# Performance work log

Measured on AMD Instinct MI355X. Metric: run time of the kernel, lower is better.

## Reference

```python
import jax, jax.numpy as jnp
import numpy as np

DIM = 384
HEADS = 8


def setup_inputs() -> dict:
    key = jax.random.key(0)
    k_x, k_qkv, k_pw, k_pb = jax.random.split(key, 4)
    x = jax.random.normal(k_x, (8, DIM, 32, 32), dtype=jnp.float32)
    # Conv2d 1x1 weights stored as [out, in]
    w_qkv = jax.random.normal(k_qkv, (3 * DIM, DIM), dtype=jnp.float32) * (DIM ** -0.5)
    w_proj = jax.random.normal(k_pw, (DIM, DIM), dtype=jnp.float32) * (DIM ** -0.5)
    b_proj = jax.random.normal(k_pb, (DIM,), dtype=jnp.float32) * 0.02
    return {"x": x, "w_qkv": w_qkv, "w_proj": w_proj, "b_proj": b_proj}


def reference(x, w_qkv, w_proj, b_proj):
    B, C, H, W = x.shape
    h = HEADS
    d = C // h
    scale = d ** -0.5
    # 1x1 conv == channel-wise linear: [B,3C,H,W]
    qkv = jnp.einsum('oc,bchw->bohw', w_qkv, x)
    q, k, v = jnp.split(qkv, 3, axis=1)
    # B (h d) H W -> B h (H W) d
    def to_heads(y):
        return y.reshape(B, h, d, H * W).transpose(0, 1, 3, 2)
    q, k, v = to_heads(q), to_heads(k), to_heads(v)
    att = jnp.einsum('bhxd,bhyd->bhxy', q * scale, k)
    att = jax.nn.softmax(att, axis=-1)
    out = jnp.einsum('bhxy,bhyd->bhxd', att, v)
    # B h (H W) d -> B (h d) H W
    out = out.transpose(0, 1, 3, 2).reshape(B, C, H, W)
    out = jnp.einsum('oc,bchw->bohw', w_proj, out) + b_proj[None, :, None, None]
    return out
```

## Files before the change

kernel.cpp:

```cpp
#include <hip/hip_runtime.h>
#include <math.h>

typedef unsigned short u16;
typedef __attribute__((ext_vector_type(8))) short short8;
typedef __attribute__((ext_vector_type(8))) unsigned short ushort8;
typedef __attribute__((ext_vector_type(4))) float floatx4;
typedef __attribute__((ext_vector_type(2))) unsigned int uint2v;
typedef __attribute__((ext_vector_type(4))) unsigned int uint4v;

#define SEQ 1024
#define CDIM 384
#define NH 8
#define DH 48
#define DP 64
#define NB 8

__device__ __forceinline__ u16 f2bf(float f){
  unsigned int u; __builtin_memcpy(&u, &f, 4);
  u = (u + 0x7fffu + ((u >> 16) & 1u)) >> 16;
  return (u16)u;
}
__device__ __forceinline__ unsigned cvtpk(float a, float b){
  unsigned r;
  asm("v_cvt_pk_bf16_f32 %0, %1, %2" : "=v"(r) : "v"(a), "v"(b));
  return r;
}
__device__ __forceinline__ void plswap32(unsigned &a, unsigned &b){
  asm("v_permlane32_swap_b32 %0, %1" : "+v"(a), "+v"(b));
}
__device__ __forceinline__ void plswap16(unsigned &a, unsigned &b){
  asm("v_permlane16_swap_b32 %0, %1" : "+v"(a), "+v"(b));
}
__device__ __forceinline__ void async16(const u16* g, u16* l){
  __builtin_amdgcn_global_load_lds((const __attribute__((address_space(1))) void*)g,
                                   (__attribute__((address_space(3))) void*)l, 16, 0, 0);
}

__global__ __launch_bounds__(256) void prep_kernel(const float* __restrict__ x,
                                                   const float* __restrict__ wq,
                                                   const float* __restrict__ wp,
                                                   u16* __restrict__ xT,
                                                   u16* __restrict__ wdst){
  __shared__ u16 ldsT[64 * 72];
  const int id = blockIdx.x;
  const int t = threadIdx.x;
  if (id < 768){
    const int bx = id & 15, by = (id >> 4) % 6, bz = id / 96;
    const int c0 = by * 64;
    const int s0 = bx * 64;
    const int rr = t >> 2, q4 = t & 3;

    const float* src = x + ((size_t)(bz * CDIM + c0 + rr)) * SEQ + s0;
#pragma unroll
    for (int i = 0; i < 4; i++){
      const int cc = q4 + i * 4;
      float4 f = *(const float4*)(src + cc * 4);
      ldsT[(cc * 4 + 0) * 72 + rr] = f2bf(f.x);
      ldsT[(cc * 4 + 1) * 72 + rr] = f2bf(f.y);
      ldsT[(cc * 4 + 2) * 72 + rr] = f2bf(f.z);
      ldsT[(cc * 4 + 3) * 72 + rr] = f2bf(f.w);
    }
    __syncthreads();
    u16* dst = xT + ((size_t)(bz * SEQ + s0 + rr)) * CDIM + c0 + q4 * 16;
    *(ushort8*)(dst)     = *(const ushort8*)&ldsT[rr * 72 + q4 * 16];
    *(ushort8*)(dst + 8) = *(const ushort8*)&ldsT[rr * 72 + q4 * 16 + 8];
  } else {
    const int NWQ = 3 * CDIM * CDIM;
    const int i = ((id - 768) * 256 + t) * 4;
    const float* src = (i < NWQ) ? (wq + i) : (wp + (i - NWQ));
    float4 f = *(const float4*)src;
    uint2v v; v[0] = cvtpk(f.x, f.y); v[1] = cvtpk(f.z, f.w);
    *(uint2v*)(wdst + i) = v;
  }
}

__global__ __launch_bounds__(256) void qkv_kernel(const u16* __restrict__ W,
                                                  const u16* __restrict__ xT,
                                                  u16* __restrict__ qws,
                                                  u16* __restrict__ kws,
                                                  u16* __restrict__ vws){
  __shared__ u16 ldsA[128 * 64];
  __shared__ u16 ldsB[64 * 64];
  const int t = threadIdx.x;
  const int w = t >> 6, l = t & 63;
  const int quad = l >> 4, li = l & 15;
  const int n0 = blockIdx.x * 64;
  const int m0 = blockIdx.y * 128;
  const int b  = blockIdx.z;

  floatx4 acc[2][4];
#pragma unroll
  for (int i = 0; i < 2; i++)
#pragma unroll
    for (int j = 0; j < 4; j++) acc[i][j] = (floatx4)0.0f;

  const u16* xb = xT + (size_t)b * SEQ * CDIM;
  const int swz = li & 7;

  for (int kk = 0; kk < CDIM; kk += 64){
    __syncthreads();
#pragma unroll
    for (int rep = 0; rep < 4; rep++){
      const int cs = rep * 256 + t;
      const int row = cs >> 3, c4 = cs & 7;
      async16(&W[(size_t)(m0 + row) * CDIM + kk + ((c4 ^ (row & 7)) << 3)], &ldsA[cs * 8]);
    }
#pragma unroll
    for (int rep = 0; rep < 2; rep++){
      const int cs = rep * 256 + t;
      const int row = cs >> 3, c4 = cs & 7;
      async16(&xb[(size_t)(n0 + row) * CDIM + kk + ((c4 ^ (row & 7)) << 3)], &ldsB[cs * 8]);
    }
    __syncthreads();
#pragma unroll
    for (int kc = 0; kc < 2; kc++){
      const int rc = ((kc * 4 + quad) ^ swz) << 3;
      short8 af[2], bf[4];
#pragma unroll
      for (int i = 0; i < 2; i++)
        af[i] = *(const short8*)&ldsA[(w * 32 + i * 16 + li) * 64 + rc];
#pragma unroll
      for (int j = 0; j < 4; j++)
        bf[j] = *(const short8*)&ldsB[(j * 16 + li) * 64 + rc];
#pragma unroll
      for (int i = 0; i < 2; i++)
#pragma unroll
        for (int j = 0; j < 4; j++)
          acc[i][j] = __builtin_amdgcn_mfma_f32_16x16x32_bf16(af[i], bf[j], acc[i][j], 0, 0, 0);
    }
  }

  const float qs = 0.14433756729740643f * 1.4426950408889634f;
  const uint2v z2 = (uint2v)0u;
#pragma unroll
  for (int i = 0; i < 2; i++){
    const int obase = m0 + w * 32 + i * 16 + quad * 4;
    const int which = obase / CDIM;
    const int rem = obase - which * CDIM;
    const int h = rem / DH;
    const int dd = rem - h * DH;
    const int pair = b * NH + h;
#pragma unroll
    for (int j = 0; j < 4; j++){
      const int s = n0 + j * 16 + li;
      floatx4 v = acc[i][j];
      if (which == 0){
        uint2v pk; pk[0] = cvtpk(v[0] * qs, v[1] * qs); pk[1] = cvtpk(v[2] * qs, v[3] * qs);
        *(uint2v*)&qws[((size_t)pair * SEQ + s) * DP + dd] = pk;
        if ((dd & 48) == 32)
          *(uint2v*)&qws[((size_t)pair * SEQ + s) * DP + dd + 16] = z2;
      } else if (which == 1){
        uint2v pk; pk[0] = cvtpk(v[0], v[1]); pk[1] = cvtpk(v[2], v[3]);
        *(uint2v*)&kws[((size_t)pair * SEQ + s) * DP + dd] = pk;
        if ((dd & 48) == 32)
          *(uint2v*)&kws[((size_t)pair * SEQ + s) * DP + dd + 16] = z2;
      } else {
#pragma unroll
        for (int r = 0; r < 4; r++)
          vws[((size_t)pair * DH + dd + r) * SEQ + s] = f2bf(v[r]);
      }
    }
  }
}

__global__ __launch_bounds__(256, 4) void attn_kernel(const u16* __restrict__ qws,
                                                      const u16* __restrict__ kws,
                                                      const u16* __restrict__ vws,
                                                      u16* __restrict__ aT){
  __shared__ u16 ldsK[2][64 * 64];
  __shared__ u16 ldsV[2][48 * 64];

  const int t = threadIdx.x;
  const int w = t >> 6, l = t & 63;
  const int quad = l >> 4, li = l & 15;
  const int id = blockIdx.x;
  const int pair = id & 63;
  const int qb = id >> 6;
  const int b = pair >> 3, h = pair & 7;
  const int qbase = qb * 64 + w * 16;
  const int swz = li & 7;

  const u16* qrow = qws + ((size_t)pair * SEQ + qbase + li) * DP;
  const short8 qf0 = *(const short8*)(qrow + quad * 8);
  const short8 qf1 = *(const short8*)(qrow + 32 + quad * 8);

  floatx4 ot[3];
#pragma unroll
  for (int dt = 0; dt < 3; dt++) ot[dt] = (floatx4)0.0f;
  float m_run = -3.0e38f, l_run = 0.0f;

  const u16* kbase = kws + (size_t)pair * SEQ * DP;
  const u16* vbase = vws + (size_t)pair * DH * SEQ;

  auto stage = [&](int kv, int pp){
#pragma unroll
    for (int rep = 0; rep < 4; rep++){
      const int cs = rep * 256 + t;
      if (cs < 512){
        const int row = cs >> 3, c4 = cs & 7;
        async16(&kbase[(size_t)(kv + row) * DP + ((c4 ^ (row & 7)) << 3)],
                &ldsK[pp][cs * 8]);
      } else if (cs < 896){
        const int cs2 = cs - 512;
        const int row = cs2 >> 3, c4 = cs2 & 7;
        async16(&vbase[(size_t)row * SEQ + kv + ((c4 ^ (row & 7)) << 3)],
                &ldsV[pp][cs2 * 8]);
      }
    }
  };

  stage(0, 0);
  for (int i = 0; i < 16; i++){
    const int p = i & 1;
    __syncthreads();
    if (i < 15) stage((i + 1) * 64, p ^ 1);

    floatx4 st[4];
#pragma unroll
    for (int yt = 0; yt < 4; yt++){
      const u16* krow = ldsK[p] + (yt * 16 + li) * 64;
      const short8 kf0 = *(const short8*)(krow + (((0 + quad) ^ swz) << 3));
      const short8 kf1 = *(const short8*)(krow + (((4 + quad) ^ swz) << 3));
      floatx4 z = (floatx4)0.0f;
      z = __builtin_amdgcn_mfma_f32_16x16x32_bf16(kf0, qf0, z, 0, 0, 0);
      z = __builtin_amdgcn_mfma_f32_16x16x32_bf16(kf1, qf1, z, 0, 0, 0);
      st[yt] = z;
    }

    float mx = -3.0e38f;
#pragma unroll
    for (int yt = 0; yt < 4; yt++)
      mx = fmaxf(mx, fmaxf(fmaxf(st[yt][0], st[yt][1]), fmaxf(st[yt][2], st[yt][3])));
    mx = fmaxf(mx, __shfl_xor(mx, 16, 64));
    mx = fmaxf(mx, __shfl_xor(mx, 32, 64));

    if (!__all(mx - m_run <= 11.0f)){
      const float mnew = fmaxf(m_run, mx);
      const float alpha = __builtin_amdgcn_exp2f(m_run - mnew);
      m_run = mnew;
      l_run *= alpha;
#pragma unroll
      for (int dt = 0; dt < 3; dt++) ot[dt] *= alpha;
    }

    unsigned wv[4][2];
    float ls = 0.0f;
#pragma unroll
    for (int yt = 0; yt < 4; yt++){
      float p0 = __builtin_amdgcn_exp2f(st[yt][0] - m_run);
      float p1 = __builtin_amdgcn_exp2f(st[yt][1] - m_run);
      float p2 = __builtin_amdgcn_exp2f(st[yt][2] - m_run);
      float p3 = __builtin_amdgcn_exp2f(st[yt][3] - m_run);
      ls += (p0 + p1) + (p2 + p3);
      wv[yt][0] = cvtpk(p0, p1);
      wv[yt][1] = cvtpk(p2, p3);
    }
    l_run += ls;

#pragma unroll
    for (int kh = 0; kh < 2; kh++){
      unsigned d0 = wv[2 * kh][0],     d1 = wv[2 * kh][1];
      unsigned e0 = wv[2 * kh + 1][0], e1 = wv[2 * kh + 1][1];
      plswap32(d0, e0); plswap16(d0, e0);
      plswap32(d1, e1); plswap16(d1, e1);
      uint4v u; u[0] = d0; u[1] = d1; u[2] = e0; u[3] = e1;
      const short8 pb = __builtin_bit_cast(short8, u);
#pragma unroll
      for (int dt = 0; dt < 3; dt++){
        const short8 vf = *(const short8*)&ldsV[p][(dt * 16 + li) * 64 +
                                                  (((kh * 4 + quad) ^ swz) << 3)];
        ot[dt] = __builtin_amdgcn_mfma_f32_16x16x32_bf16(vf, pb, ot[dt], 0, 0, 0);
      }
    }
  }

  float ls = l_run;
  ls += __shfl_xor(ls, 16, 64);
  ls += __shfl_xor(ls, 32, 64);
  const float rl = __builtin_amdgcn_rcpf(ls);
  const int q = qbase + li;
#pragma unroll
  for (int dt = 0; dt < 3; dt++){
    floatx4 v = ot[dt];
    uint2v pk; pk[0] = cvtpk(v[0] * rl, v[1] * rl); pk[1] = cvtpk(v[2] * rl, v[3] * rl);
    *(uint2v*)&aT[((size_t)b * SEQ + q) * CDIM + h * DH + dt * 16 + quad * 4] = pk;
  }
}

__global__ __launch_bounds__(256) void proj_kernel(const u16* __restrict__ W,
                                                   const u16* __restrict__ aT,
                                                   const float* __restrict__ bias,
                                                   float* __restrict__ out){
  __shared__ u16 ldsA[128 * 64];
  __shared__ u16 ldsB[64 * 64];
  const int t = threadIdx.x;
  const int w = t >> 6, l = t & 63;
  const int quad = l >> 4, li = l & 15;
  const int n0 = blockIdx.x * 64;
  const int m0 = blockIdx.y * 128;
  const int b  = blockIdx.z;

  floatx4 acc[2][4];
#pragma unroll
  for (int i = 0; i < 2; i++)
#pragma unroll
    for (int j = 0; j < 4; j++) acc[i][j] = (floatx4)0.0f;

  const u16* ab = aT + (size_t)b * SEQ * CDIM;
  const int swz = li & 7;

  for (int kk = 0; kk < CDIM; kk += 64){
    __syncthreads();
#pragma unroll
    for (int rep = 0; rep < 4; rep++){
      const int cs = rep * 256 + t;
      const int row = cs >> 3, c4 = cs & 7;
      async16(&W[(size_t)(m0 + row) * CDIM + kk + ((c4 ^ (row & 7)) << 3)], &ldsA[cs * 8]);
    }
#pragma unroll
    for (int rep = 0; rep < 2; rep++){
      const int cs = rep * 256 + t;
      const int row = cs >> 3, c4 = cs & 7;
      async16(&ab[(size_t)(n0 + row) * CDIM + kk + ((c4 ^ (row & 7)) << 3)], &ldsB[cs * 8]);
    }
    __syncthreads();
#pragma unroll
    for (int kc = 0; kc < 2; kc++){
      const int rc = ((kc * 4 + quad) ^ swz) << 3;
      short8 af[2], bf[4];
#pragma unroll
      for (int i = 0; i < 2; i++)
        af[i] = *(const short8*)&ldsA[(w * 32 + i * 16 + li) * 64 + rc];
#pragma unroll
      for (int j = 0; j < 4; j++)
        bf[j] = *(const short8*)&ldsB[(j * 16 + li) * 64 + rc];
#pragma unroll
      for (int i = 0; i < 2; i++)
#pragma unroll
        for (int j = 0; j < 4; j++)
          acc[i][j] = __builtin_amdgcn_mfma_f32_16x16x32_bf16(af[i], bf[j], acc[i][j], 0, 0, 0);
    }
  }

#pragma unroll
  for (int i = 0; i < 2; i++){
    const int o0 = m0 + w * 32 + i * 16 + quad * 4;
    float bs[4];
#pragma unroll
    for (int r = 0; r < 4; r++) bs[r] = bias[o0 + r];
#pragma unroll
    for (int j = 0; j < 4; j++){
      const int s = n0 + j * 16 + li;
#pragma unroll
      for (int r = 0; r < 4; r++)
        out[((size_t)b * CDIM + o0 + r) * SEQ + s] = acc[i][j][r] + bs[r];
    }
  }
}

extern "C" void kernel_launch(void* const* d_in, const int* in_sizes, int n_in,
                              void* d_out, int out_size, void* d_ws, size_t ws_size,
                              hipStream_t stream) {
  const float* x      = (const float*)d_in[0];
  const float* w_qkv  = (const float*)d_in[1];
  const float* w_proj = (const float*)d_in[2];
  const float* b_proj = (const float*)d_in[3];
  float* out = (float*)d_out;

  char* ws = (char*)d_ws;
  const size_t SZX = (size_t)NB * SEQ * CDIM * sizeof(u16);
  const size_t SZQ = (size_t)NB * NH * SEQ * DP * sizeof(u16);
  const size_t SZV = (size_t)NB * NH * SEQ * DH * sizeof(u16);
  u16* xT   = (u16*)(ws);
  u16* qws  = (u16*)(ws + SZX);
  u16* kws  = (u16*)(ws + SZX + SZQ);
  u16* vws  = (u16*)(ws + SZX + 2 * SZQ);
  u16* wq_b = (u16*)(ws + SZX + 2 * SZQ + SZV);
  u16* wp_b = wq_b + (size_t)3 * CDIM * CDIM;
  u16* aT   = xT;

  prep_kernel<<<dim3(768 + 576), 256, 0, stream>>>(x, w_qkv, w_proj, xT, wq_b);
  qkv_kernel<<<dim3(16, 9, 8), 256, 0, stream>>>(wq_b, xT, qws, kws, vws);
  attn_kernel<<<dim3(1024), 256, 0, stream>>>(qws, kws, vws, aT);
  proj_kernel<<<dim3(16, 3, 8), 256, 0, stream>>>(wp_b, aT, b_proj, out);
}
```

Baseline: 122.7 us.

## Process two query tiles per wave in attention to reuse K/V fragments

Each wave now handles 32 query rows (two 16-row MFMA tiles) instead of 16, so every K and V fragment read from LDS feeds two MFMAs, and each block covers 128 queries. The grid shrinks from 1024 to 512 blocks, which halves the K/V global staging traffic per query. s_setprio hints are added around the MFMA sections. In exchange, register pressure roughly doubles, launch bounds drop to 2 waves per SIMD, and with 512 blocks on 256 CUs the machine has less parallelism to hide latency.

New measurement: 121.8 us. About the same (-0.7%).

```diff
diff --git a/kernel.cpp b/kernel.cpp
--- a/kernel.cpp
+++ b/kernel.cpp
@@ -163,7 +163,7 @@
   }
 }
 
-__global__ __launch_bounds__(256, 4) void attn_kernel(const u16* __restrict__ qws,
+__global__ __launch_bounds__(256, 2) void attn_kernel(const u16* __restrict__ qws,
                                                       const u16* __restrict__ kws,
                                                       const u16* __restrict__ vws,
                                                       u16* __restrict__ aT){
@@ -177,17 +177,21 @@
   const int pair = id & 63;
   const int qb = id >> 6;
   const int b = pair >> 3, h = pair & 7;
-  const int qbase = qb * 64 + w * 16;
+  const int qbase = qb * 128 + w * 32;
   const int swz = li & 7;
 
-  const u16* qrow = qws + ((size_t)pair * SEQ + qbase + li) * DP;
-  const short8 qf0 = *(const short8*)(qrow + quad * 8);
-  const short8 qf1 = *(const short8*)(qrow + 32 + quad * 8);
-
-  floatx4 ot[3];
-#pragma unroll
-  for (int dt = 0; dt < 3; dt++) ot[dt] = (floatx4)0.0f;
-  float m_run = -3.0e38f, l_run = 0.0f;
+  const u16* qrow0 = qws + ((size_t)pair * SEQ + qbase + li) * DP;
+  const u16* qrow1 = qrow0 + 16 * DP;
+  const short8 qfA0 = *(const short8*)(qrow0 + quad * 8);
+  const short8 qfA1 = *(const short8*)(qrow0 + 32 + quad * 8);
+  const short8 qfB0 = *(const short8*)(qrow1 + quad * 8);
+  const short8 qfB1 = *(const short8*)(qrow1 + 32 + quad * 8);
+
+  floatx4 ot0[3], ot1[3];
+#pragma unroll
+  for (int dt = 0; dt < 3; dt++){ ot0[dt] = (floatx4)0.0f; ot1[dt] = (floatx4)0.0f; }
+  float m0 = -3.0e38f, l0 = 0.0f;
+  float m1 = -3.0e38f, l1 = 0.0f;
 
   const u16* kbase = kws + (size_t)pair * SEQ * DP;
   const u16* vbase = vws + (size_t)pair * DH * SEQ;
@@ -215,75 +219,102 @@
     __syncthreads();
     if (i < 15) stage((i + 1) * 64, p ^ 1);
 
-    floatx4 st[4];
+    floatx4 st0[4], st1[4];
+    __builtin_amdgcn_s_setprio(1);
 #pragma unroll
     for (int yt = 0; yt < 4; yt++){
       const u16* krow = ldsK[p] + (yt * 16 + li) * 64;
       const short8 kf0 = *(const short8*)(krow + (((0 + quad) ^ swz) << 3));
       const short8 kf1 = *(const short8*)(krow + (((4 + quad) ^ swz) << 3));
-      floatx4 z = (floatx4)0.0f;
-      z = __builtin_amdgcn_mfma_f32_16x16x32_bf16(kf0, qf0, z, 0, 0, 0);
-      z = __builtin_amdgcn_mfma_f32_16x16x32_bf16(kf1, qf1, z, 0, 0, 0);
-      st[yt] = z;
-    }
-
-    float mx = -3.0e38f;
-#pragma unroll
-    for (int yt = 0; yt < 4; yt++)
-      mx = fmaxf(mx, fmaxf(fmaxf(st[yt][0], st[yt][1]), fmaxf(st[yt][2], st[yt][3])));
-    mx = fmaxf(mx, __shfl_xor(mx, 16, 64));
-    mx = fmaxf(mx, __shfl_xor(mx, 32, 64));
-
-    if (!__all(mx - m_run <= 11.0f)){
-      const float mnew = fmaxf(m_run, mx);
-      const float alpha = __builtin_amdgcn_exp2f(m_run - mnew);
-      m_run = mnew;
-      l_run *= alpha;
-#pragma unroll
-      for (int dt = 0; dt < 3; dt++) ot[dt] *= alpha;
-    }
-
-    unsigned wv[4][2];
-    float ls = 0.0f;
+      floatx4 z0 = (floatx4)0.0f, z1 = (floatx4)0.0f;
+      z0 = __builtin_amdgcn_mfma_f32_16x16x32_bf16(kf0, qfA0, z0, 0, 0, 0);
+      z1 = __builtin_amdgcn_mfma_f32_16x16x32_bf16(kf0, qfB0, z1, 0, 0, 0);
+      z0 = __builtin_amdgcn_mfma_f32_16x16x32_bf16(kf1, qfA1, z0, 0, 0, 0);
+      z1 = __builtin_amdgcn_mfma_f32_16x16x32_bf16(kf1, qfB1, z1, 0, 0, 0);
+      st0[yt] = z0; st1[yt] = z1;
+    }
+    __builtin_amdgcn_s_setprio(0);
+
+    float mx0 = -3.0e38f, mx1 = -3.0e38f;
 #pragma unroll
     for (int yt = 0; yt < 4; yt++){
-      float p0 = __builtin_amdgcn_exp2f(st[yt][0] - m_run);
-      float p1 = __builtin_amdgcn_exp2f(st[yt][1] - m_run);
-      float p2 = __builtin_amdgcn_exp2f(st[yt][2] - m_run);
-      float p3 = __builtin_amdgcn_exp2f(st[yt][3] - m_run);
-      ls += (p0 + p1) + (p2 + p3);
-      wv[yt][0] = cvtpk(p0, p1);
-      wv[yt][1] = cvtpk(p2, p3);
-    }
-    l_run += ls;
-
+      mx0 = fmaxf(mx0, fmaxf(fmaxf(st0[yt][0], st0[yt][1]), fmaxf(st0[yt][2], st0[yt][3])));
+      mx1 = fmaxf(mx1, fmaxf(fmaxf(st1[yt][0], st1[yt][1]), fmaxf(st1[yt][2], st1[yt][3])));
+    }
+    mx0 = fmaxf(mx0, __shfl_xor(mx0, 16, 64));
+    mx0 = fmaxf(mx0, __shfl_xor(mx0, 32, 64));
+    mx1 = fmaxf(mx1, __shfl_xor(mx1, 16, 64));
+    mx1 = fmaxf(mx1, __shfl_xor(mx1, 32, 64));
+
+    if (!__all((mx0 - m0 <= 11.0f) & (mx1 - m1 <= 11.0f))){
+      const float n0 = fmaxf(m0, mx0), n1 = fmaxf(m1, mx1);
+      const float a0 = __builtin_amdgcn_exp2f(m0 - n0);
+      const float a1 = __builtin_amdgcn_exp2f(m1 - n1);
+      m0 = n0; m1 = n1;
+      l0 *= a0; l1 *= a1;
+#pragma unroll
+      for (int dt = 0; dt < 3; dt++){ ot0[dt] *= a0; ot1[dt] *= a1; }
+    }
+
+    unsigned wv0[4][2], wv1[4][2];
+    float ls0 = 0.0f, ls1 = 0.0f;
+#pragma unroll
+    for (int yt = 0; yt < 4; yt++){
+      float a = __builtin_amdgcn_exp2f(st0[yt][0] - m0);
+      float bq = __builtin_amdgcn_exp2f(st0[yt][1] - m0);
+      float c = __builtin_amdgcn_exp2f(st0[yt][2] - m0);
+      float d = __builtin_amdgcn_exp2f(st0[yt][3] - m0);
+      ls0 += (a + bq) + (c + d);
+      wv0[yt][0] = cvtpk(a, bq); wv0[yt][1] = cvtpk(c, d);
+      float e = __builtin_amdgcn_exp2f(st1[yt][0] - m1);
+      float f = __builtin_amdgcn_exp2f(st1[yt][1] - m1);
+      float g = __builtin_amdgcn_exp2f(st1[yt][2] - m1);
+      float hh = __builtin_amdgcn_exp2f(st1[yt][3] - m1);
+      ls1 += (e + f) + (g + hh);
+      wv1[yt][0] = cvtpk(e, f); wv1[yt][1] = cvtpk(g, hh);
+    }
+    l0 += ls0; l1 += ls1;
+
+    __builtin_amdgcn_s_setprio(1);
 #pragma unroll
     for (int kh = 0; kh < 2; kh++){
-      unsigned d0 = wv[2 * kh][0],     d1 = wv[2 * kh][1];
-      unsigned e0 = wv[2 * kh + 1][0], e1 = wv[2 * kh + 1][1];
+      unsigned d0 = wv0[2 * kh][0],     d1 = wv0[2 * kh][1];
+      unsigned e0 = wv0[2 * kh + 1][0], e1 = wv0[2 * kh + 1][1];
       plswap32(d0, e0); plswap16(d0, e0);
       plswap32(d1, e1); plswap16(d1, e1);
-      uint4v u; u[0] = d0; u[1] = d1; u[2] = e0; u[3] = e1;
-      const short8 pb = __builtin_bit_cast(short8, u);
+      uint4v u0; u0[0] = d0; u0[1] = d1; u0[2] = e0; u0[3] = e1;
+      const short8 pb0 = __builtin_bit_cast(short8, u0);
+      unsigned f0 = wv1[2 * kh][0],     f1 = wv1[2 * kh][1];
+      unsigned g0 = wv1[2 * kh + 1][0], g1 = wv1[2 * kh + 1][1];
+      plswap32(f0, g0); plswap16(f0, g0);
+      plswap32(f1, g1); plswap16(f1, g1);
+      uint4v u1; u1[0] = f0; u1[1] = f1; u1[2] = g0; u1[3] = g1;
+      const short8 pb1 = __builtin_bit_cast(short8, u1);
 #pragma unroll
       for (int dt = 0; dt < 3; dt++){
         const short8 vf = *(const short8*)&ldsV[p][(dt * 16 + li) * 64 +
                                                   (((kh * 4 + quad) ^ swz) << 3)];
-        ot[dt] = __builtin_amdgcn_mfma_f32_16x16x32_bf16(vf, pb, ot[dt], 0, 0, 0);
+        ot0[dt] = __builtin_amdgcn_mfma_f32_16x16x32_bf16(vf, pb0, ot0[dt], 0, 0, 0);
+        ot1[dt] = __builtin_amdgcn_mfma_f32_16x16x32_bf16(vf, pb1, ot1[dt], 0, 0, 0);
       }
     }
-  }
-
-  float ls = l_run;
-  ls += __shfl_xor(ls, 16, 64);
-  ls += __shfl_xor(ls, 32, 64);
-  const float rl = __builtin_amdgcn_rcpf(ls);
-  const int q = qbase + li;
+    __builtin_amdgcn_s_setprio(0);
+  }
+
+  float s0 = l0, s1 = l1;
+  s0 += __shfl_xor(s0, 16, 64); s0 += __shfl_xor(s0, 32, 64);
+  s1 += __shfl_xor(s1, 16, 64); s1 += __shfl_xor(s1, 32, 64);
+  const float rl0 = __builtin_amdgcn_rcpf(s0);
+  const float rl1 = __builtin_amdgcn_rcpf(s1);
+  const int q0 = qbase + li;
 #pragma unroll
   for (int dt = 0; dt < 3; dt++){
-    floatx4 v = ot[dt];
-    uint2v pk; pk[0] = cvtpk(v[0] * rl, v[1] * rl); pk[1] = cvtpk(v[2] * rl, v[3] * rl);
-    *(uint2v*)&aT[((size_t)b * SEQ + q) * CDIM + h * DH + dt * 16 + quad * 4] = pk;
+    floatx4 v = ot0[dt];
+    uint2v pk; pk[0] = cvtpk(v[0] * rl0, v[1] * rl0); pk[1] = cvtpk(v[2] * rl0, v[3] * rl0);
+    *(uint2v*)&aT[((size_t)b * SEQ + q0) * CDIM + h * DH + dt * 16 + quad * 4] = pk;
+    floatx4 v1 = ot1[dt];
+    uint2v pk1; pk1[0] = cvtpk(v1[0] * rl1, v1[1] * rl1); pk1[1] = cvtpk(v1[2] * rl1, v1[3] * rl1);
+    *(uint2v*)&aT[((size_t)b * SEQ + q0 + 16) * CDIM + h * DH + dt * 16 + quad * 4] = pk1;
   }
 }
 
@@ -381,6 +412,6 @@
 
   prep_kernel<<<dim3(768 + 576), 256, 0, stream>>>(x, w_qkv, w_proj, xT, wq_b);
   qkv_kernel<<<dim3(16, 9, 8), 256, 0, stream>>>(wq_b, xT, qws, kws, vws);
-  attn_kernel<<<dim3(1024), 256, 0, stream>>>(qws, kws, vws, aT);
+  attn_kernel<<<dim3(512), 256, 0, stream>>>(qws, kws, vws, aT);
   proj_kernel<<<dim3(16, 3, 8), 256, 0, stream>>>(wp_b, aT, b_proj, out);
 }
```
